# Kernel tuning notes

Measured on AMD Instinct MI355X. Metric: run time of the kernel, lower is better.

## Reference

```python
import jax, jax.numpy as jnp
import numpy as np

LAMB = 0.01       # self.lamb
CASCADES = 3

# Forward difference D along `axis` with zero last row: (Dv)[i] = v[i+1]-v[i], (Dv)[N-1]=0.
# This is exactly the sparse matvec matmul(Dx, v.view(-1)).reshape(v.shape), batched.
def fwd_diff(v, axis):
    d = jnp.diff(v, axis=axis)
    pad = [(0, 0)] * v.ndim
    pad[axis] = (0, 1)
    return jnp.pad(d, pad)

# Exact adjoint D^T: (D^T p)[0] = -p[0]; (D^T p)[j] = p[j-1]-p[j]; (D^T p)[N-1] = p[N-2].
def fwd_diff_t(p, axis):
    n = p.shape[axis]
    pad_front = [(0, 0)] * p.ndim
    pad_front[axis] = (1, 0)
    a = jax.lax.slice_in_dim(jnp.pad(p, pad_front), 0, n, axis=axis)   # a[j] = p[j-1], a[0]=0
    pad_back = [(0, 0)] * p.ndim
    pad_back[axis] = (0, 1)
    b = jnp.pad(jax.lax.slice_in_dim(p, 0, n - 1, axis=axis), pad_back)  # b[j]=p[j], b[N-1]=0
    return a - b

def dual_prox(x, sig):
    # Dual AE block: clip onto [-sigma, sigma] ball (TV dual proximal)
    return jnp.clip(x, -sig, sig)

def setup_inputs() -> dict:
    key = jax.random.key(0)
    k1, k2 = jax.random.split(key)
    B, D, H, W = 2, 256, 256, 128
    image = jax.random.normal(k1, (B, D, H, W), dtype=jnp.float32)
    sino = jax.random.normal(k2, (B, D, H, W), dtype=jnp.float32)
    sigma = jnp.ones((4,), dtype=jnp.float32)
    nt = jnp.zeros((CASCADES,), dtype=jnp.float32)
    return {"image": image, "sino": sino, "sigma": sigma, "nt": nt}

def reference(image, sino, sigma, nt):
    t = image
    outs = [t]
    p = jnp.zeros_like(image)
    q = jnp.zeros_like(image)
    s = jnp.zeros_like(image)
    for c in range(CASCADES):
        # ITE (BeijingGeometry stand-in): data-fidelity gradient step
        z = t - LAMB * (t - sino)
        pnew = dual_prox(p - fwd_diff(z, 1), sigma[0])
        qnew = dual_prox(q - fwd_diff(z, 2), sigma[1])
        snew = dual_prox(s - fwd_diff(z, 3), sigma[2])
        znew = dual_prox(z, sigma[3])
        # momentum extrapolation
        p = pnew + nt[c] * (pnew - p)
        q = qnew + nt[c] * (qnew - q)
        s = snew + nt[c] * (snew - s)
        # divergence via adjoint stencils + primal update
        t = fwd_diff_t(p, 1) + fwd_diff_t(q, 2) + fwd_diff_t(s, 3) + znew
        outs.append(t)
    return tuple(outs)
```

## Files before the change

kernel.cpp:

```cpp
#include <hip/hip_runtime.h>

#define LAMB 0.01f
constexpr int Bc = 2, Dc = 256, Hc = 256, Wc = 128;
constexpr int HWc = Hc * Wc;
constexpr int NELEM = Bc * Dc * HWc;

constexpr int TD = 8, TH = 8, TW = 32;
constexpr int RD = TD + 6, RH = TH + 6, RW = TW + 6;
constexpr int RWP = 40;
constexpr int NROWS = RD * RH;
constexpr int NTHR = 1024;
constexpr int GDt = Dc / TD, GHt = Hc / TH, GWt = Wc / TW;
constexpr int NBLK = Bc * GDt * GHt * GWt;

static_assert(4 * NROWS * RWP * 4 <= 160 * 1024, "LDS over 160 KiB");
static_assert(NBLK % 8 == 0, "swizzle needs nblk % 8 == 0");

typedef float f4 __attribute__((ext_vector_type(4)));

__device__ __forceinline__ float clipf(float x, float s) {
    return fminf(fmaxf(x, -s), s);
}
__device__ __forceinline__ float zof(float t, float s) { return t + LAMB * (s - t); }
__device__ __forceinline__ float dual_up(float pold, float dz, float sg, float ntc) {
    float pn = clipf(pold - dz, sg);
    return pn + ntc * (pn - pold);
}

__global__ __launch_bounds__(NTHR) void fused3(
    const float* __restrict__ image, const float* __restrict__ sino,
    float* __restrict__ out0, float* __restrict__ out1,
    float* __restrict__ out2, float* __restrict__ out3,
    const float* __restrict__ sigma, const float* __restrict__ nt)
{
    __shared__ float Z[NROWS * RWP];
    __shared__ float P[NROWS * RWP];
    __shared__ float Q[NROWS * RWP];
    __shared__ float S[NROWS * RWP];

    int bid = (int)blockIdx.x;
    bid = (bid & 7) * (NBLK >> 3) + (bid >> 3);
    const int wT = bid & (GWt - 1);
    const int hT = (bid >> 2) & (GHt - 1);
    const int dT = (bid >> 7) & (GDt - 1);
    const int b  = bid >> 12;
    const int d0 = dT * TD, h0 = hT * TH, w0 = wT * TW;
    const int base = b * Dc * HWc;

    const float s0 = sigma[0], s1 = sigma[1], s2 = sigma[2], s3 = sigma[3];
    const int tid = (int)threadIdx.x;

    for (int t = tid; t < NROWS * 10; t += NTHR) {
        const int row = t / 10, g = t - row * 10;
        const int rd = row / RH, rh = row - rd * RH;
        const int gd = d0 - 3 + rd, gh = h0 - 3 + rh;
        const bool rowok = ((unsigned)gd < (unsigned)Dc) && ((unsigned)gh < (unsigned)Hc);
        const int rbase = base + gd * HWc + gh * Wc;
        f4 z;
#pragma unroll
        for (int k = 0; k < 4; ++k) {
            const int gw = w0 - 3 + g * 4 + k;
            float v = 0.f;
            if (rowok && (unsigned)gw < (unsigned)Wc) {
                const int gix = rbase + gw;
                v = zof(image[gix], sino[gix]);
            }
            z[k] = v;
        }
        *(f4*)&Z[row * RWP + g * 4] = z;
    }
    for (int t = tid; t < TD * TH * (TW / 4); t += NTHR) {
        const int g = t & (TW / 4 - 1);
        const int r = t >> 3;
        const int td = r >> 3, th = r & 7;
        const int gix = base + (d0 + td) * HWc + (h0 + th) * Wc + w0 + g * 4;
        __builtin_nontemporal_store(*(const f4*)&image[gix], (f4*)&out0[gix]);
    }
    __syncthreads();

#pragma unroll
    for (int c = 0; c < 3; ++c) {
        const float ntc = nt[c];

        for (int t = tid; t < 169 * 10; t += NTHR) {
            const int row13 = t / 10, g = t - row13 * 10;
            const int rd = row13 / 13, rh = row13 - (row13 / 13) * 13;
            const int li = (rd * RH + rh) * RWP + g * 4;

            const f4 zc4 = *(const f4*)&Z[li];
            const float z5 = (g < 9) ? Z[li + 4] : 0.f;
            const f4 zd4 = *(const f4*)&Z[li + RH * RWP];
            const f4 zh4 = *(const f4*)&Z[li + RWP];

            f4 po = {0.f, 0.f, 0.f, 0.f}, qo = po, so = po;
            if (c > 0) {
                po = *(const f4*)&P[li];
                qo = *(const f4*)&Q[li];
                so = *(const f4*)&S[li];
            }
            const int gd = d0 - 3 + rd, gh = h0 - 3 + rh;
            const bool dok = (unsigned)gd < (unsigned)Dc;
            const bool hok = (unsigned)gh < (unsigned)Hc;
            const bool dlast = (gd == Dc - 1), hlast = (gh == Hc - 1);

            f4 pn, qn, sn;
#pragma unroll
            for (int k = 0; k < 4; ++k) {
                const int gw = w0 - 3 + g * 4 + k;
                const bool inb = dok && hok && ((unsigned)gw < (unsigned)Wc);
                const float zck = zc4[k];
                const float zr  = (k == 3) ? z5 : zc4[k + 1];
                const float dzD = dlast ? 0.f : (zd4[k] - zck);
                const float dzH = hlast ? 0.f : (zh4[k] - zck);
                const float dzW = (gw == Wc - 1) ? 0.f : (zr - zck);
                pn[k] = inb ? dual_up(po[k], dzD, s0, ntc) : 0.f;
                qn[k] = inb ? dual_up(qo[k], dzH, s1, ntc) : 0.f;
                sn[k] = inb ? dual_up(so[k], dzW, s2, ntc) : 0.f;
            }
            *(f4*)&P[li] = pn;
            *(f4*)&Q[li] = qn;
            *(f4*)&S[li] = sn;
        }
        __syncthreads();

        float* outc = (c == 0) ? out1 : ((c == 1) ? out2 : out3);
        for (int t = tid; t < 144 * 10; t += NTHR) {
            const int row12 = t / 10, g = t - row12 * 10;
            const int rdm = row12 / 12;
            const int rd = 1 + rdm, rh = 1 + (row12 - rdm * 12);
            const int li = (rd * RH + rh) * RWP + g * 4;

            const f4 pc = *(const f4*)&P[li];
            const f4 pm = *(const f4*)&P[li - RH * RWP];
            const f4 qc = *(const f4*)&Q[li];
            const f4 qm = *(const f4*)&Q[li - RWP];
            const f4 sc = *(const f4*)&S[li];
            const float sm1 = S[li - 1];
            const f4 zc4 = *(const f4*)&Z[li];

            float tn[4];
#pragma unroll
            for (int k = 0; k < 4; ++k) {
                const float smk = (k == 0) ? sm1 : sc[k - 1];
                tn[k] = (pm[k] - pc[k]) + (qm[k] - qc[k]) + (smk - sc[k])
                      + clipf(zc4[k], s3);
            }

            const int gd = d0 - 3 + rd, gh = h0 - 3 + rh;
            const int rix = base + gd * HWc + gh * Wc;
            const bool tilerow = (rd >= 3 && rd < 3 + TD && rh >= 3 && rh < 3 + TH);
            if (tilerow) {
#pragma unroll
                for (int k = 0; k < 4; ++k) {
                    const int rw = g * 4 + k;
                    if (rw >= 3 && rw < 3 + TW)
                        __builtin_nontemporal_store(tn[k], &outc[rix + (w0 - 3 + rw)]);
                }
            }
            if (c < 2) {
                const bool dhok = ((unsigned)gd < (unsigned)Dc) && ((unsigned)gh < (unsigned)Hc);
                f4 zn;
#pragma unroll
                for (int k = 0; k < 4; ++k) {
                    const int gw = w0 - 3 + g * 4 + k;
                    const bool inb = dhok && ((unsigned)gw < (unsigned)Wc);
                    zn[k] = inb ? zof(tn[k], sino[rix + gw]) : 0.f;
                }
                *(f4*)&Z[li] = zn;
            }
        }
        __syncthreads();
    }
}

extern "C" void kernel_launch(void* const* d_in, const int* in_sizes, int n_in,
                              void* d_out, int out_size, void* d_ws, size_t ws_size,
                              hipStream_t stream) {
    const float* image = (const float*)d_in[0];
    const float* sino  = (const float*)d_in[1];
    const float* sigma = (const float*)d_in[2];
    const float* nt    = (const float*)d_in[3];

    float* out  = (float*)d_out;
    fused3<<<dim3(NBLK), dim3(NTHR), 0, stream>>>(
        image, sino,
        out, out + (size_t)NELEM, out + 2 * (size_t)NELEM, out + 3 * (size_t)NELEM,
        sigma, nt);
}
```

Baseline: 722.5 us.

## Specialize interior tiles, align halo for vector IO, shrink per-cascade compute regions

The fused three-cascade kernel is split into templated interior and boundary paths. Interior tiles skip all bounds and last-row checks and use aligned float4 global loads and stores, made possible by shifting the LDS halo to start four columns left (row pitch 44). Each cascade now computes only the shrinking region it actually needs instead of a fixed 13x13 or 12x12 halo, which cuts redundant LDS and ALU work. The costs are larger code size from template duplication, slightly more LDS per block, and the chance of divergence or register pressure differences between the two paths.

```diff
diff --git a/kernel.cpp b/kernel.cpp
--- a/kernel.cpp
+++ b/kernel.cpp
@@ -6,14 +6,16 @@
 constexpr int NELEM = Bc * Dc * HWc;
 
 constexpr int TD = 8, TH = 8, TW = 32;
-constexpr int RD = TD + 6, RH = TH + 6, RW = TW + 6;
-constexpr int RWP = 40;
-constexpr int NROWS = RD * RH;
+constexpr int RDm = TD + 6, RHm = TH + 6;
+constexpr int RW = 4 + TW + 3;
+constexpr int RWP = 44;
+constexpr int NROWS = RDm * RHm;
 constexpr int NTHR = 1024;
 constexpr int GDt = Dc / TD, GHt = Hc / TH, GWt = Wc / TW;
 constexpr int NBLK = Bc * GDt * GHt * GWt;
-
-static_assert(4 * NROWS * RWP * 4 <= 160 * 1024, "LDS over 160 KiB");
+constexpr int LSZ = NROWS * RWP;
+
+static_assert(4 * LSZ * 4 <= 160 * 1024, "LDS over 160 KiB");
 static_assert(NBLK % 8 == 0, "swizzle needs nblk % 8 == 0");
 
 typedef float f4 __attribute__((ext_vector_type(4)));
@@ -25,6 +27,192 @@
 __device__ __forceinline__ float dual_up(float pold, float dz, float sg, float ntc) {
     float pn = clipf(pold - dz, sg);
     return pn + ntc * (pn - pold);
+}
+
+template <int C, bool INT>
+__device__ __forceinline__ void dual_pass(
+    float* __restrict__ Z, float* __restrict__ P, float* __restrict__ Q,
+    float* __restrict__ S, int d0, int h0, int w0,
+    float s0, float s1, float s2, float ntc)
+{
+    constexpr int R0 = C, NR = 13 - 2 * C;
+    constexpr int NG = (C == 2) ? 9 : 10;
+    constexpr int NIT = NR * NR * NG;
+    for (int it = (int)threadIdx.x; it < NIT; it += NTHR) {
+        const int row = it / NG, g = it - row * NG;
+        const int r2 = row / NR;
+        const int rd = R0 + r2, rh = R0 + (row - r2 * NR);
+        const int li = (rd * RHm + rh) * RWP + g * 4;
+
+        const f4 zc = *(const f4*)&Z[li];
+        const float z5 = Z[li + 4];
+        const f4 zd = *(const f4*)&Z[li + RHm * RWP];
+        const f4 zh = *(const f4*)&Z[li + RWP];
+
+        f4 po = {0.f, 0.f, 0.f, 0.f}, qo = po, so = po;
+        if (C > 0) {
+            po = *(const f4*)&P[li];
+            qo = *(const f4*)&Q[li];
+            so = *(const f4*)&S[li];
+        }
+        f4 pn, qn, sn;
+        if (INT) {
+#pragma unroll
+            for (int k = 0; k < 4; ++k) {
+                const float zr = (k == 3) ? z5 : zc[k + 1];
+                pn[k] = dual_up(po[k], zd[k] - zc[k], s0, ntc);
+                qn[k] = dual_up(qo[k], zh[k] - zc[k], s1, ntc);
+                sn[k] = dual_up(so[k], zr - zc[k], s2, ntc);
+            }
+        } else {
+            const int gd = d0 - 3 + rd, gh = h0 - 3 + rh;
+            const bool dok = (unsigned)gd < (unsigned)Dc;
+            const bool hok = (unsigned)gh < (unsigned)Hc;
+            const bool dlast = (gd == Dc - 1), hlast = (gh == Hc - 1);
+#pragma unroll
+            for (int k = 0; k < 4; ++k) {
+                const int gw = w0 - 4 + g * 4 + k;
+                const bool inb = dok && hok && ((unsigned)gw < (unsigned)Wc);
+                const float zr = (k == 3) ? z5 : zc[k + 1];
+                const float dzD = dlast ? 0.f : (zd[k] - zc[k]);
+                const float dzH = hlast ? 0.f : (zh[k] - zc[k]);
+                const float dzW = (gw == Wc - 1) ? 0.f : (zr - zc[k]);
+                pn[k] = inb ? dual_up(po[k], dzD, s0, ntc) : 0.f;
+                qn[k] = inb ? dual_up(qo[k], dzH, s1, ntc) : 0.f;
+                sn[k] = inb ? dual_up(so[k], dzW, s2, ntc) : 0.f;
+            }
+        }
+        *(f4*)&P[li] = pn;
+        *(f4*)&Q[li] = qn;
+        *(f4*)&S[li] = sn;
+    }
+}
+
+template <int C, bool INT>
+__device__ __forceinline__ void t_pass(
+    const float* __restrict__ sino, float* __restrict__ outc,
+    float* __restrict__ Z, float* __restrict__ P, float* __restrict__ Q,
+    float* __restrict__ S, int base, int d0, int h0, int w0, float s3)
+{
+    constexpr int T0 = C + 1, NR = 12 - 2 * C;
+    constexpr int G0 = (C == 2) ? 1 : 0;
+    constexpr int NG = (C == 2) ? 8 : 10;
+    constexpr int NIT = NR * NR * NG;
+    for (int it = (int)threadIdx.x; it < NIT; it += NTHR) {
+        const int row = it / NG, g = G0 + (it - row * NG);
+        const int r2 = row / NR;
+        const int rd = T0 + r2, rh = T0 + (row - r2 * NR);
+        const int li = (rd * RHm + rh) * RWP + g * 4;
+
+        const f4 pc = *(const f4*)&P[li];
+        const f4 pm = *(const f4*)&P[li - RHm * RWP];
+        const f4 qc = *(const f4*)&Q[li];
+        const f4 qm = *(const f4*)&Q[li - RWP];
+        const f4 sc = *(const f4*)&S[li];
+        const float sm1 = S[li - 1];
+        const f4 zc = *(const f4*)&Z[li];
+
+        f4 tn;
+#pragma unroll
+        for (int k = 0; k < 4; ++k) {
+            const float smk = (k == 0) ? sm1 : sc[k - 1];
+            tn[k] = (pm[k] - pc[k]) + (qm[k] - qc[k]) + (smk - sc[k])
+                  + clipf(zc[k], s3);
+        }
+
+        const int gd = d0 - 3 + rd, gh = h0 - 3 + rh;
+        const int rix = base + gd * HWc + gh * Wc + (w0 - 4 + g * 4);
+        const bool tile = (C == 2) ||
+            (((unsigned)(rd - 3) < (unsigned)TD) &&
+             ((unsigned)(rh - 3) < (unsigned)TH) &&
+             ((unsigned)(g - 1) < 8u));
+        if (tile)
+            __builtin_nontemporal_store(tn, (f4*)&outc[rix]);
+
+        if (C < 2) {
+            f4 zn;
+            if (INT) {
+                const f4 sn4 = *(const f4*)&sino[rix];
+#pragma unroll
+                for (int k = 0; k < 4; ++k) zn[k] = zof(tn[k], sn4[k]);
+            } else {
+                const bool dhok = ((unsigned)gd < (unsigned)Dc) &&
+                                  ((unsigned)gh < (unsigned)Hc);
+#pragma unroll
+                for (int k = 0; k < 4; ++k) {
+                    const int gw = w0 - 4 + g * 4 + k;
+                    const bool inb = dhok && ((unsigned)gw < (unsigned)Wc);
+                    zn[k] = inb ? zof(tn[k], sino[rix + k]) : 0.f;
+                }
+            }
+            *(f4*)&Z[li] = zn;
+        }
+    }
+}
+
+template <bool INT>
+__device__ __forceinline__ void run_block(
+    const float* __restrict__ image, const float* __restrict__ sino,
+    float* __restrict__ out0, float* __restrict__ out1,
+    float* __restrict__ out2, float* __restrict__ out3,
+    const float* __restrict__ sigma, const float* __restrict__ nt,
+    float* __restrict__ Z, float* __restrict__ P, float* __restrict__ Q,
+    float* __restrict__ S, int base, int d0, int h0, int w0)
+{
+    const int tid = (int)threadIdx.x;
+    const float s0 = sigma[0], s1 = sigma[1], s2 = sigma[2], s3 = sigma[3];
+
+    for (int it = tid; it < NROWS * 10; it += NTHR) {
+        const int row = it / 10, g = it - row * 10;
+        const int rd = row / RHm, rh = row - (row / RHm) * RHm;
+        const int gd = d0 - 3 + rd, gh = h0 - 3 + rh;
+        const int li = row * RWP + g * 4;
+        if (INT) {
+            const int gix = base + gd * HWc + gh * Wc + (w0 - 4 + g * 4);
+            const f4 a = *(const f4*)&image[gix];
+            const f4 b = *(const f4*)&sino[gix];
+            f4 z;
+#pragma unroll
+            for (int k = 0; k < 4; ++k) z[k] = zof(a[k], b[k]);
+            *(f4*)&Z[li] = z;
+        } else {
+            const bool rowok = ((unsigned)gd < (unsigned)Dc) &&
+                               ((unsigned)gh < (unsigned)Hc);
+            const int rbase = base + gd * HWc + gh * Wc;
+            f4 z;
+#pragma unroll
+            for (int k = 0; k < 4; ++k) {
+                const int gw = w0 - 4 + g * 4 + k;
+                float v = 0.f;
+                if (rowok && (unsigned)gw < (unsigned)Wc)
+                    v = zof(image[rbase + gw], sino[rbase + gw]);
+                z[k] = v;
+            }
+            *(f4*)&Z[li] = z;
+        }
+    }
+    for (int it = tid; it < TD * TH * (TW / 4); it += NTHR) {
+        const int g = it & 7;
+        const int r = it >> 3;
+        const int td = r >> 3, th = r & 7;
+        const int gix = base + (d0 + td) * HWc + (h0 + th) * Wc + w0 + g * 4;
+        __builtin_nontemporal_store(*(const f4*)&image[gix], (f4*)&out0[gix]);
+    }
+    __syncthreads();
+
+    const float nt0 = nt[0], nt1 = nt[1], nt2 = nt[2];
+
+    dual_pass<0, INT>(Z, P, Q, S, d0, h0, w0, s0, s1, s2, nt0);
+    __syncthreads();
+    t_pass<0, INT>(sino, out1, Z, P, Q, S, base, d0, h0, w0, s3);
+    __syncthreads();
+    dual_pass<1, INT>(Z, P, Q, S, d0, h0, w0, s0, s1, s2, nt1);
+    __syncthreads();
+    t_pass<1, INT>(sino, out2, Z, P, Q, S, base, d0, h0, w0, s3);
+    __syncthreads();
+    dual_pass<2, INT>(Z, P, Q, S, d0, h0, w0, s0, s1, s2, nt2);
+    __syncthreads();
+    t_pass<2, INT>(sino, out3, Z, P, Q, S, base, d0, h0, w0, s3);
 }
 
 __global__ __launch_bounds__(NTHR) void fused3(
@@ -33,10 +221,10 @@
     float* __restrict__ out2, float* __restrict__ out3,
     const float* __restrict__ sigma, const float* __restrict__ nt)
 {
-    __shared__ float Z[NROWS * RWP];
-    __shared__ float P[NROWS * RWP];
-    __shared__ float Q[NROWS * RWP];
-    __shared__ float S[NROWS * RWP];
+    __shared__ float Z[LSZ];
+    __shared__ float P[LSZ];
+    __shared__ float Q[LSZ];
+    __shared__ float S[LSZ];
 
     int bid = (int)blockIdx.x;
     bid = (bid & 7) * (NBLK >> 3) + (bid >> 3);
@@ -47,130 +235,15 @@
     const int d0 = dT * TD, h0 = hT * TH, w0 = wT * TW;
     const int base = b * Dc * HWc;
 
-    const float s0 = sigma[0], s1 = sigma[1], s2 = sigma[2], s3 = sigma[3];
-    const int tid = (int)threadIdx.x;
-
-    for (int t = tid; t < NROWS * 10; t += NTHR) {
-        const int row = t / 10, g = t - row * 10;
-        const int rd = row / RH, rh = row - rd * RH;
-        const int gd = d0 - 3 + rd, gh = h0 - 3 + rh;
-        const bool rowok = ((unsigned)gd < (unsigned)Dc) && ((unsigned)gh < (unsigned)Hc);
-        const int rbase = base + gd * HWc + gh * Wc;
-        f4 z;
-#pragma unroll
-        for (int k = 0; k < 4; ++k) {
-            const int gw = w0 - 3 + g * 4 + k;
-            float v = 0.f;
-            if (rowok && (unsigned)gw < (unsigned)Wc) {
-                const int gix = rbase + gw;
-                v = zof(image[gix], sino[gix]);
-            }
-            z[k] = v;
-        }
-        *(f4*)&Z[row * RWP + g * 4] = z;
-    }
-    for (int t = tid; t < TD * TH * (TW / 4); t += NTHR) {
-        const int g = t & (TW / 4 - 1);
-        const int r = t >> 3;
-        const int td = r >> 3, th = r & 7;
-        const int gix = base + (d0 + td) * HWc + (h0 + th) * Wc + w0 + g * 4;
-        __builtin_nontemporal_store(*(const f4*)&image[gix], (f4*)&out0[gix]);
-    }
-    __syncthreads();
-
-#pragma unroll
-    for (int c = 0; c < 3; ++c) {
-        const float ntc = nt[c];
-
-        for (int t = tid; t < 169 * 10; t += NTHR) {
-            const int row13 = t / 10, g = t - row13 * 10;
-            const int rd = row13 / 13, rh = row13 - (row13 / 13) * 13;
-            const int li = (rd * RH + rh) * RWP + g * 4;
-
-            const f4 zc4 = *(const f4*)&Z[li];
-            const float z5 = (g < 9) ? Z[li + 4] : 0.f;
-            const f4 zd4 = *(const f4*)&Z[li + RH * RWP];
-            const f4 zh4 = *(const f4*)&Z[li + RWP];
-
-            f4 po = {0.f, 0.f, 0.f, 0.f}, qo = po, so = po;
-            if (c > 0) {
-                po = *(const f4*)&P[li];
-                qo = *(const f4*)&Q[li];
-                so = *(const f4*)&S[li];
-            }
-            const int gd = d0 - 3 + rd, gh = h0 - 3 + rh;
-            const bool dok = (unsigned)gd < (unsigned)Dc;
-            const bool hok = (unsigned)gh < (unsigned)Hc;
-            const bool dlast = (gd == Dc - 1), hlast = (gh == Hc - 1);
-
-            f4 pn, qn, sn;
-#pragma unroll
-            for (int k = 0; k < 4; ++k) {
-                const int gw = w0 - 3 + g * 4 + k;
-                const bool inb = dok && hok && ((unsigned)gw < (unsigned)Wc);
-                const float zck = zc4[k];
-                const float zr  = (k == 3) ? z5 : zc4[k + 1];
-                const float dzD = dlast ? 0.f : (zd4[k] - zck);
-                const float dzH = hlast ? 0.f : (zh4[k] - zck);
-                const float dzW = (gw == Wc - 1) ? 0.f : (zr - zck);
-                pn[k] = inb ? dual_up(po[k], dzD, s0, ntc) : 0.f;
-                qn[k] = inb ? dual_up(qo[k], dzH, s1, ntc) : 0.f;
-                sn[k] = inb ? dual_up(so[k], dzW, s2, ntc) : 0.f;
-            }
-            *(f4*)&P[li] = pn;
-            *(f4*)&Q[li] = qn;
-            *(f4*)&S[li] = sn;
-        }
-        __syncthreads();
-
-        float* outc = (c == 0) ? out1 : ((c == 1) ? out2 : out3);
-        for (int t = tid; t < 144 * 10; t += NTHR) {
-            const int row12 = t / 10, g = t - row12 * 10;
-            const int rdm = row12 / 12;
-            const int rd = 1 + rdm, rh = 1 + (row12 - rdm * 12);
-            const int li = (rd * RH + rh) * RWP + g * 4;
-
-            const f4 pc = *(const f4*)&P[li];
-            const f4 pm = *(const f4*)&P[li - RH * RWP];
-            const f4 qc = *(const f4*)&Q[li];
-            const f4 qm = *(const f4*)&Q[li - RWP];
-            const f4 sc = *(const f4*)&S[li];
-            const float sm1 = S[li - 1];
-            const f4 zc4 = *(const f4*)&Z[li];
-
-            float tn[4];
-#pragma unroll
-            for (int k = 0; k < 4; ++k) {
-                const float smk = (k == 0) ? sm1 : sc[k - 1];
-                tn[k] = (pm[k] - pc[k]) + (qm[k] - qc[k]) + (smk - sc[k])
-                      + clipf(zc4[k], s3);
-            }
-
-            const int gd = d0 - 3 + rd, gh = h0 - 3 + rh;
-            const int rix = base + gd * HWc + gh * Wc;
-            const bool tilerow = (rd >= 3 && rd < 3 + TD && rh >= 3 && rh < 3 + TH);
-            if (tilerow) {
-#pragma unroll
-                for (int k = 0; k < 4; ++k) {
-                    const int rw = g * 4 + k;
-                    if (rw >= 3 && rw < 3 + TW)
-                        __builtin_nontemporal_store(tn[k], &outc[rix + (w0 - 3 + rw)]);
-                }
-            }
-            if (c < 2) {
-                const bool dhok = ((unsigned)gd < (unsigned)Dc) && ((unsigned)gh < (unsigned)Hc);
-                f4 zn;
-#pragma unroll
-                for (int k = 0; k < 4; ++k) {
-                    const int gw = w0 - 3 + g * 4 + k;
-                    const bool inb = dhok && ((unsigned)gw < (unsigned)Wc);
-                    zn[k] = inb ? zof(tn[k], sino[rix + gw]) : 0.f;
-                }
-                *(f4*)&Z[li] = zn;
-            }
-        }
-        __syncthreads();
-    }
+    const bool interior = (dT >= 1) && (dT <= GDt - 2) &&
+                          (hT >= 1) && (hT <= GHt - 2) &&
+                          (wT >= 1) && (wT <= GWt - 2);
+    if (interior)
+        run_block<true>(image, sino, out0, out1, out2, out3, sigma, nt,
+                        Z, P, Q, S, base, d0, h0, w0);
+    else
+        run_block<false>(image, sino, out0, out1, out2, out3, sigma, nt,
+                         Z, P, Q, S, base, d0, h0, w0);
 }
 
 extern "C" void kernel_launch(void* const* d_in, const int* in_sizes, int n_in,
@@ -181,7 +254,7 @@
     const float* sigma = (const float*)d_in[2];
     const float* nt    = (const float*)d_in[3];
 
-    float* out  = (float*)d_out;
+    float* out = (float*)d_out;
     fused3<<<dim3(NBLK), dim3(NTHR), 0, stream>>>(
         image, sino,
         out, out + (size_t)NELEM, out + 2 * (size_t)NELEM, out + 3 * (size_t)NELEM,
```

After: 608.2 us. 15.8% less time.

## Keep per-cell state in registers, shrink halo per cascade, specialize interior blocks

Applied to the files above, without the earlier changes.

The kernel is restructured so each thread owns up to two fixed cells and keeps z, p, q, s and the sino values in registers across all three cascades. This removes repeated LDS reloads and the global reloads of sino. The halo is realigned to 4-wide groups so global loads and stores become aligned f4 accesses, and the active region shrinks with each cascade to skip dead halo work. Interior blocks get a template path without boundary checks. In exchange, register pressure rises at 1024 threads per block, and the row padding goes from 40 to 44 floats, which grows LDS.

```diff
diff --git a/kernel.cpp b/kernel.cpp
--- a/kernel.cpp
+++ b/kernel.cpp
@@ -6,14 +6,17 @@
 constexpr int NELEM = Bc * Dc * HWc;
 
 constexpr int TD = 8, TH = 8, TW = 32;
-constexpr int RD = TD + 6, RH = TH + 6, RW = TW + 6;
-constexpr int RWP = 40;
-constexpr int NROWS = RD * RH;
+constexpr int RDm = TD + 6, RHm = TH + 6;
+constexpr int RWP = 44;
+constexpr int NROWS = RDm * RHm;
+constexpr int NGRP = 10;
+constexpr int NCELL = NROWS * NGRP;
 constexpr int NTHR = 1024;
 constexpr int GDt = Dc / TD, GHt = Hc / TH, GWt = Wc / TW;
 constexpr int NBLK = Bc * GDt * GHt * GWt;
-
-static_assert(4 * NROWS * RWP * 4 <= 160 * 1024, "LDS over 160 KiB");
+constexpr int LSZ = NROWS * RWP;
+
+static_assert(4 * LSZ * 4 <= 160 * 1024, "LDS over 160 KiB");
 static_assert(NBLK % 8 == 0, "swizzle needs nblk % 8 == 0");
 
 typedef float f4 __attribute__((ext_vector_type(4)));
@@ -22,9 +25,157 @@
     return fminf(fmaxf(x, -s), s);
 }
 __device__ __forceinline__ float zof(float t, float s) { return t + LAMB * (s - t); }
-__device__ __forceinline__ float dual_up(float pold, float dz, float sg, float ntc) {
-    float pn = clipf(pold - dz, sg);
-    return pn + ntc * (pn - pold);
+__device__ __forceinline__ float dual_up(float po, float dz, float sg, float ntc) {
+    float pn = clipf(po - dz, sg);
+    return pn + ntc * (pn - po);
+}
+
+struct Cell {
+    f4 z, p, q, s, sn;
+    int li, rix;
+    int rd, rh, g;
+    int gd, gh, gwb;
+};
+
+template <bool INT>
+__device__ __forceinline__ void run_block(
+    const float* __restrict__ image, const float* __restrict__ sino,
+    float* __restrict__ out0, float* __restrict__ out1,
+    float* __restrict__ out2, float* __restrict__ out3,
+    const float* __restrict__ sigma, const float* __restrict__ nt,
+    float* __restrict__ Zs, float* __restrict__ Ps, float* __restrict__ Qs,
+    float* __restrict__ Ss, int base, int d0, int h0, int w0)
+{
+    const int tid = (int)threadIdx.x;
+    const float s0 = sigma[0], s1 = sigma[1], s2 = sigma[2], s3 = sigma[3];
+
+    auto initCell = [&](int cIdx, Cell& cl) {
+        const int row = cIdx / NGRP;
+        cl.g   = cIdx - row * NGRP;
+        cl.rd  = row / RHm;
+        cl.rh  = row - cl.rd * RHm;
+        cl.li  = row * RWP + cl.g * 4;
+        cl.gd  = d0 - 3 + cl.rd;
+        cl.gh  = h0 - 3 + cl.rh;
+        cl.gwb = w0 - 4 + cl.g * 4;
+        cl.rix = base + cl.gd * HWc + cl.gh * Wc + cl.gwb;
+        cl.p = (f4){0.f, 0.f, 0.f, 0.f};
+        cl.q = cl.p; cl.s = cl.p;
+        f4 av;
+        if (INT) {
+            av    = *(const f4*)&image[cl.rix];
+            cl.sn = *(const f4*)&sino[cl.rix];
+#pragma unroll
+            for (int k = 0; k < 4; ++k) cl.z[k] = zof(av[k], cl.sn[k]);
+        } else {
+            const bool rowok = ((unsigned)cl.gd < (unsigned)Dc) &&
+                               ((unsigned)cl.gh < (unsigned)Hc);
+#pragma unroll
+            for (int k = 0; k < 4; ++k) {
+                const bool inb = rowok && ((unsigned)(cl.gwb + k) < (unsigned)Wc);
+                float a = 0.f, b = 0.f;
+                if (inb) { a = image[cl.rix + k]; b = sino[cl.rix + k]; }
+                av[k] = a; cl.sn[k] = b;
+                cl.z[k] = inb ? zof(a, b) : 0.f;
+            }
+        }
+        *(f4*)&Zs[cl.li] = cl.z;
+        const bool tile = ((unsigned)(cl.rd - 3) < (unsigned)TD) &&
+                          ((unsigned)(cl.rh - 3) < (unsigned)TH) &&
+                          ((unsigned)(cl.g - 1) < 8u);
+        if (tile) __builtin_nontemporal_store(av, (f4*)&out0[cl.rix]);
+    };
+
+    auto dual = [&](Cell& cl, int C, int NGd, float ntc) {
+        if (cl.rd < C || cl.rd >= 13 - C || cl.rh < C || cl.rh >= 13 - C ||
+            cl.g >= NGd) return;
+        const f4 zd   = *(const f4*)&Zs[cl.li + RHm * RWP];
+        const f4 zh   = *(const f4*)&Zs[cl.li + RWP];
+        const float z5 = Zs[cl.li + 4];
+        if (INT) {
+#pragma unroll
+            for (int k = 0; k < 4; ++k) {
+                const float zr = (k == 3) ? z5 : cl.z[k + 1];
+                cl.p[k] = dual_up(cl.p[k], zd[k] - cl.z[k], s0, ntc);
+                cl.q[k] = dual_up(cl.q[k], zh[k] - cl.z[k], s1, ntc);
+                cl.s[k] = dual_up(cl.s[k], zr - cl.z[k], s2, ntc);
+            }
+        } else {
+            const bool dok = (unsigned)cl.gd < (unsigned)Dc;
+            const bool hok = (unsigned)cl.gh < (unsigned)Hc;
+            const bool dlast = (cl.gd == Dc - 1), hlast = (cl.gh == Hc - 1);
+#pragma unroll
+            for (int k = 0; k < 4; ++k) {
+                const int gw = cl.gwb + k;
+                const bool inb = dok && hok && ((unsigned)gw < (unsigned)Wc);
+                const float zr = (k == 3) ? z5 : cl.z[k + 1];
+                const float dzD = dlast ? 0.f : (zd[k] - cl.z[k]);
+                const float dzH = hlast ? 0.f : (zh[k] - cl.z[k]);
+                const float dzW = (gw == Wc - 1) ? 0.f : (zr - cl.z[k]);
+                cl.p[k] = inb ? dual_up(cl.p[k], dzD, s0, ntc) : 0.f;
+                cl.q[k] = inb ? dual_up(cl.q[k], dzH, s1, ntc) : 0.f;
+                cl.s[k] = inb ? dual_up(cl.s[k], dzW, s2, ntc) : 0.f;
+            }
+        }
+        *(f4*)&Ps[cl.li] = cl.p;
+        *(f4*)&Qs[cl.li] = cl.q;
+        *(f4*)&Ss[cl.li] = cl.s;
+    };
+
+    auto tpass = [&](Cell& cl, int C, int G0, int G1, float* __restrict__ outc,
+                     bool updZ) {
+        if (cl.rd <= C || cl.rd >= 13 - C || cl.rh <= C || cl.rh >= 13 - C ||
+            cl.g < G0 || cl.g >= G1) return;
+        const f4 pm    = *(const f4*)&Ps[cl.li - RHm * RWP];
+        const f4 qm    = *(const f4*)&Qs[cl.li - RWP];
+        const float sm1 = Ss[cl.li - 1];
+        f4 tn;
+#pragma unroll
+        for (int k = 0; k < 4; ++k) {
+            const float smk = (k == 0) ? sm1 : cl.s[k - 1];
+            tn[k] = (pm[k] - cl.p[k]) + (qm[k] - cl.q[k]) + (smk - cl.s[k])
+                  + clipf(cl.z[k], s3);
+        }
+        const bool tile = ((unsigned)(cl.rd - 3) < (unsigned)TD) &&
+                          ((unsigned)(cl.rh - 3) < (unsigned)TH) &&
+                          ((unsigned)(cl.g - 1) < 8u);
+        if (tile) __builtin_nontemporal_store(tn, (f4*)&outc[cl.rix]);
+        if (updZ) {
+            if (INT) {
+#pragma unroll
+                for (int k = 0; k < 4; ++k) cl.z[k] = zof(tn[k], cl.sn[k]);
+            } else {
+                const bool dhok = ((unsigned)cl.gd < (unsigned)Dc) &&
+                                  ((unsigned)cl.gh < (unsigned)Hc);
+#pragma unroll
+                for (int k = 0; k < 4; ++k) {
+                    const bool inb = dhok && ((unsigned)(cl.gwb + k) < (unsigned)Wc);
+                    cl.z[k] = inb ? zof(tn[k], cl.sn[k]) : 0.f;
+                }
+            }
+            *(f4*)&Zs[cl.li] = cl.z;
+        }
+    };
+
+    Cell cA, cB;
+    const bool two = (tid + NTHR) < NCELL;
+    initCell(tid, cA);
+    if (two) initCell(tid + NTHR, cB);
+    __syncthreads();
+
+    const float nt0 = nt[0], nt1 = nt[1], nt2 = nt[2];
+
+    dual(cA, 0, 10, nt0); if (two) dual(cB, 0, 10, nt0);
+    __syncthreads();
+    tpass(cA, 0, 0, 10, out1, true); if (two) tpass(cB, 0, 0, 10, out1, true);
+    __syncthreads();
+    dual(cA, 1, 10, nt1); if (two) dual(cB, 1, 10, nt1);
+    __syncthreads();
+    tpass(cA, 1, 0, 10, out2, true); if (two) tpass(cB, 1, 0, 10, out2, true);
+    __syncthreads();
+    dual(cA, 2, 9, nt2); if (two) dual(cB, 2, 9, nt2);
+    __syncthreads();
+    tpass(cA, 2, 1, 9, out3, false); if (two) tpass(cB, 2, 1, 9, out3, false);
 }
 
 __global__ __launch_bounds__(NTHR) void fused3(
@@ -33,10 +184,10 @@
     float* __restrict__ out2, float* __restrict__ out3,
     const float* __restrict__ sigma, const float* __restrict__ nt)
 {
-    __shared__ float Z[NROWS * RWP];
-    __shared__ float P[NROWS * RWP];
-    __shared__ float Q[NROWS * RWP];
-    __shared__ float S[NROWS * RWP];
+    __shared__ float Zs[LSZ];
+    __shared__ float Ps[LSZ];
+    __shared__ float Qs[LSZ];
+    __shared__ float Ss[LSZ];
 
     int bid = (int)blockIdx.x;
     bid = (bid & 7) * (NBLK >> 3) + (bid >> 3);
@@ -47,130 +198,15 @@
     const int d0 = dT * TD, h0 = hT * TH, w0 = wT * TW;
     const int base = b * Dc * HWc;
 
-    const float s0 = sigma[0], s1 = sigma[1], s2 = sigma[2], s3 = sigma[3];
-    const int tid = (int)threadIdx.x;
-
-    for (int t = tid; t < NROWS * 10; t += NTHR) {
-        const int row = t / 10, g = t - row * 10;
-        const int rd = row / RH, rh = row - rd * RH;
-        const int gd = d0 - 3 + rd, gh = h0 - 3 + rh;
-        const bool rowok = ((unsigned)gd < (unsigned)Dc) && ((unsigned)gh < (unsigned)Hc);
-        const int rbase = base + gd * HWc + gh * Wc;
-        f4 z;
-#pragma unroll
-        for (int k = 0; k < 4; ++k) {
-            const int gw = w0 - 3 + g * 4 + k;
-            float v = 0.f;
-            if (rowok && (unsigned)gw < (unsigned)Wc) {
-                const int gix = rbase + gw;
-                v = zof(image[gix], sino[gix]);
-            }
-            z[k] = v;
-        }
-        *(f4*)&Z[row * RWP + g * 4] = z;
-    }
-    for (int t = tid; t < TD * TH * (TW / 4); t += NTHR) {
-        const int g = t & (TW / 4 - 1);
-        const int r = t >> 3;
-        const int td = r >> 3, th = r & 7;
-        const int gix = base + (d0 + td) * HWc + (h0 + th) * Wc + w0 + g * 4;
-        __builtin_nontemporal_store(*(const f4*)&image[gix], (f4*)&out0[gix]);
-    }
-    __syncthreads();
-
-#pragma unroll
-    for (int c = 0; c < 3; ++c) {
-        const float ntc = nt[c];
-
-        for (int t = tid; t < 169 * 10; t += NTHR) {
-            const int row13 = t / 10, g = t - row13 * 10;
-            const int rd = row13 / 13, rh = row13 - (row13 / 13) * 13;
-            const int li = (rd * RH + rh) * RWP + g * 4;
-
-            const f4 zc4 = *(const f4*)&Z[li];
-            const float z5 = (g < 9) ? Z[li + 4] : 0.f;
-            const f4 zd4 = *(const f4*)&Z[li + RH * RWP];
-            const f4 zh4 = *(const f4*)&Z[li + RWP];
-
-            f4 po = {0.f, 0.f, 0.f, 0.f}, qo = po, so = po;
-            if (c > 0) {
-                po = *(const f4*)&P[li];
-                qo = *(const f4*)&Q[li];
-                so = *(const f4*)&S[li];
-            }
-            const int gd = d0 - 3 + rd, gh = h0 - 3 + rh;
-            const bool dok = (unsigned)gd < (unsigned)Dc;
-            const bool hok = (unsigned)gh < (unsigned)Hc;
-            const bool dlast = (gd == Dc - 1), hlast = (gh == Hc - 1);
-
-            f4 pn, qn, sn;
-#pragma unroll
-            for (int k = 0; k < 4; ++k) {
-                const int gw = w0 - 3 + g * 4 + k;
-                const bool inb = dok && hok && ((unsigned)gw < (unsigned)Wc);
-                const float zck = zc4[k];
-                const float zr  = (k == 3) ? z5 : zc4[k + 1];
-                const float dzD = dlast ? 0.f : (zd4[k] - zck);
-                const float dzH = hlast ? 0.f : (zh4[k] - zck);
-                const float dzW = (gw == Wc - 1) ? 0.f : (zr - zck);
-                pn[k] = inb ? dual_up(po[k], dzD, s0, ntc) : 0.f;
-                qn[k] = inb ? dual_up(qo[k], dzH, s1, ntc) : 0.f;
-                sn[k] = inb ? dual_up(so[k], dzW, s2, ntc) : 0.f;
-            }
-            *(f4*)&P[li] = pn;
-            *(f4*)&Q[li] = qn;
-            *(f4*)&S[li] = sn;
-        }
-        __syncthreads();
-
-        float* outc = (c == 0) ? out1 : ((c == 1) ? out2 : out3);
-        for (int t = tid; t < 144 * 10; t += NTHR) {
-            const int row12 = t / 10, g = t - row12 * 10;
-            const int rdm = row12 / 12;
-            const int rd = 1 + rdm, rh = 1 + (row12 - rdm * 12);
-            const int li = (rd * RH + rh) * RWP + g * 4;
-
-            const f4 pc = *(const f4*)&P[li];
-            const f4 pm = *(const f4*)&P[li - RH * RWP];
-            const f4 qc = *(const f4*)&Q[li];
-            const f4 qm = *(const f4*)&Q[li - RWP];
-            const f4 sc = *(const f4*)&S[li];
-            const float sm1 = S[li - 1];
-            const f4 zc4 = *(const f4*)&Z[li];
-
-            float tn[4];
-#pragma unroll
-            for (int k = 0; k < 4; ++k) {
-                const float smk = (k == 0) ? sm1 : sc[k - 1];
-                tn[k] = (pm[k] - pc[k]) + (qm[k] - qc[k]) + (smk - sc[k])
-                      + clipf(zc4[k], s3);
-            }
-
-            const int gd = d0 - 3 + rd, gh = h0 - 3 + rh;
-            const int rix = base + gd * HWc + gh * Wc;
-            const bool tilerow = (rd >= 3 && rd < 3 + TD && rh >= 3 && rh < 3 + TH);
-            if (tilerow) {
-#pragma unroll
-                for (int k = 0; k < 4; ++k) {
-                    const int rw = g * 4 + k;
-                    if (rw >= 3 && rw < 3 + TW)
-                        __builtin_nontemporal_store(tn[k], &outc[rix + (w0 - 3 + rw)]);
-                }
-            }
-            if (c < 2) {
-                const bool dhok = ((unsigned)gd < (unsigned)Dc) && ((unsigned)gh < (unsigned)Hc);
-                f4 zn;
-#pragma unroll
-                for (int k = 0; k < 4; ++k) {
-                    const int gw = w0 - 3 + g * 4 + k;
-                    const bool inb = dhok && ((unsigned)gw < (unsigned)Wc);
-                    zn[k] = inb ? zof(tn[k], sino[rix + gw]) : 0.f;
-                }
-                *(f4*)&Z[li] = zn;
-            }
-        }
-        __syncthreads();
-    }
+    const bool interior = (dT >= 1) && (dT <= GDt - 2) &&
+                          (hT >= 1) && (hT <= GHt - 2) &&
+                          (wT >= 1) && (wT <= GWt - 2);
+    if (interior)
+        run_block<true>(image, sino, out0, out1, out2, out3, sigma, nt,
+                        Zs, Ps, Qs, Ss, base, d0, h0, w0);
+    else
+        run_block<false>(image, sino, out0, out1, out2, out3, sigma, nt,
+                         Zs, Ps, Qs, Ss, base, d0, h0, w0);
 }
 
 extern "C" void kernel_launch(void* const* d_in, const int* in_sizes, int n_in,
@@ -181,7 +217,7 @@
     const float* sigma = (const float*)d_in[2];
     const float* nt    = (const float*)d_in[3];
 
-    float* out  = (float*)d_out;
+    float* out = (float*)d_out;
     fused3<<<dim3(NBLK), dim3(NTHR), 0, stream>>>(
         image, sino,
         out, out + (size_t)NELEM, out + 2 * (size_t)NELEM, out + 3 * (size_t)NELEM,
```

New measurement: 581.7 us. -19.5%, faster.
